# Kernel optimization log

Measured on AMD Instinct MI355X. Metric: run time of the kernel, lower is better.

The kernel has to match this reference:

```python
import jax, jax.numpy as jnp
import numpy as np

N_EMBED = 1024
HIDDEN = int(2 / 3 * 4 * N_EMBED)  # 2730, matches SwiGLU default
NUM_EXPERTS = 8
TOP_K = 2


def setup_inputs() -> dict:
    key = jax.random.key(0)
    ks = jax.random.split(key, 5)
    B, T, C, E, H = 2, 2048, N_EMBED, NUM_EXPERTS, HIDDEN
    s = 0.02
    return {
        "x": jax.random.normal(ks[0], (B, T, C), dtype=jnp.float32),
        "gate_w": jax.random.normal(ks[1], (E, C), dtype=jnp.float32) * s,  # Linear(C->E) weight [out,in]
        "w1": jax.random.normal(ks[2], (E, H, C), dtype=jnp.float32) * s,   # per-expert Linear(C->H)
        "w2": jax.random.normal(ks[3], (E, H, C), dtype=jnp.float32) * s,   # per-expert Linear(C->H)
        "w3": jax.random.normal(ks[4], (E, C, H), dtype=jnp.float32) * s,   # per-expert Linear(H->C)
    }


def reference(x, gate_w, w1, w2, w3):
    B, T, C = x.shape
    E = gate_w.shape[0]
    xt = x.reshape(-1, C)                      # [N, C], N = B*T
    N = xt.shape[0]

    # Router: top-k logits, softmax over the selected logits only
    logits = jnp.einsum("nc,ec->ne", xt, gate_w)          # [N, E]
    top_vals, top_idx = jax.lax.top_k(logits, TOP_K)       # [N, K]
    top_w = jax.nn.softmax(top_vals.astype(jnp.float32), axis=-1).astype(x.dtype)

    # Dense routing-weight matrix [N, E] (top-k indices are distinct per token)
    route = jnp.zeros((N, E), dtype=x.dtype)
    route = route.at[jnp.arange(N)[:, None], top_idx].set(top_w)

    # SwiGLU for all experts, batched over the expert axis (faithful math,
    # vectorized instead of the per-expert Python-loop gather/scatter)
    h1 = jnp.einsum("nc,ehc->enh", xt, w1)                 # [E, N, H]
    h2 = jnp.einsum("nc,ehc->enh", xt, w2)                 # [E, N, H]
    act = jax.nn.silu(h1) * h2                              # [E, N, H]
    expert_out = jnp.einsum("enh,ech->enc", act, w3)       # [E, N, C]

    out = jnp.einsum("ne,enc->nc", route, expert_out)      # weighted combine
    return out.reshape(B, T, C)
```

## Files before the change

### kernel.cpp

```cpp
#include <hip/hip_runtime.h>
#include <hip/hip_bf16.h>
#include <cstdint>
#include <cstddef>

#define TOKENS 4096
#define CDIM   1024
#define HDIM   2730
#define HPAD2  2816
#define NEXP   8
#define NPAIR  (TOKENS * 2)
#define NTB1   (HPAD2 / 64)
#define NTB2   (CDIM / 128)

typedef __bf16 bf16_t;
typedef bf16_t bf16x8 __attribute__((ext_vector_type(8)));
typedef float  f32x4  __attribute__((ext_vector_type(4)));

static __device__ __forceinline__ unsigned short f2bf(float f) {
    union { float f; unsigned int u; } v; v.f = f;
    unsigned int u = v.u;
    return (unsigned short)((u + 0x7FFFu + ((u >> 16) & 1u)) >> 16);
}
static __device__ __forceinline__ unsigned int pack2(float a, float b) {
    return (unsigned int)f2bf(a) | ((unsigned int)f2bf(b) << 16);
}

typedef __attribute__((address_space(3))) unsigned int lds_uint;
typedef const __attribute__((address_space(1))) unsigned int glob_uint;
static __device__ __forceinline__ void gl_lds16(const void* g, void* l) {
    __builtin_amdgcn_global_load_lds((glob_uint*)g, (lds_uint*)l, 16, 0, 0);
}


__global__ void moe_init(int* meta) {
    if (threadIdx.x < 64) meta[threadIdx.x] = 0;
}

__global__ __launch_bounds__(256) void moe_router(
    const float* __restrict__ x, const float* __restrict__ gw,
    int* __restrict__ meta, int* __restrict__ tok_idx, float* __restrict__ tok_w)
{
    int wave = threadIdx.x >> 6;
    int lane = threadIdx.x & 63;
    int t = blockIdx.x * 4 + wave;

    float acc[NEXP];
#pragma unroll
    for (int e = 0; e < NEXP; ++e) acc[e] = 0.f;

    const float4* xr = (const float4*)(x + (size_t)t * CDIM);
#pragma unroll
    for (int it = 0; it < 4; ++it) {
        int c4 = it * 64 + lane;
        float4 xv = xr[c4];
#pragma unroll
        for (int e = 0; e < NEXP; ++e) {
            float4 gv = ((const float4*)(gw + e * CDIM))[c4];
            acc[e] += xv.x * gv.x + xv.y * gv.y + xv.z * gv.z + xv.w * gv.w;
        }
    }
#pragma unroll
    for (int e = 0; e < NEXP; ++e) {
#pragma unroll
        for (int off = 32; off > 0; off >>= 1)
            acc[e] += __shfl_xor(acc[e], off, 64);
    }
    if (lane == 0) {
        int e0 = 0; float v0 = acc[0];
#pragma unroll
        for (int e = 1; e < NEXP; ++e) if (acc[e] > v0) { v0 = acc[e]; e0 = e; }
        int e1 = -1; float v1 = -3.0e38f;
#pragma unroll
        for (int e = 0; e < NEXP; ++e) if (e != e0 && acc[e] > v1) { v1 = acc[e]; e1 = e; }
        float w0 = 1.f / (1.f + __expf(v1 - v0));
        tok_idx[2 * t] = e0; tok_idx[2 * t + 1] = e1;
        tok_w[2 * t] = w0;  tok_w[2 * t + 1] = 1.f - w0;
        atomicAdd(&meta[e0], 1);
        atomicAdd(&meta[e1], 1);
    }
}

__global__ void moe_scan(int* meta) {
    if (threadIdx.x == 0) {
        int s = 0;
        for (int e = 0; e < NEXP; ++e) { meta[8 + e] = s; s += meta[e]; }
        meta[16] = s;
        int nb = 0;
        for (int e = 0; e < NEXP; ++e) {
            int beg = meta[8 + e], end = meta[8 + e] + meta[e];
            for (int m0 = beg; m0 < end; m0 += 128) {
                meta[32 + 2 * nb] = e;
                meta[33 + 2 * nb] = m0;
                ++nb;
            }
        }
        meta[17] = nb;
    }
}

__global__ __launch_bounds__(256) void moe_scatter(
    const int* __restrict__ tok_idx, const float* __restrict__ tok_w, int* meta,
    int* __restrict__ pair_token, float* __restrict__ pair_w)
{
    int t = blockIdx.x * 256 + threadIdx.x;
    if (t >= TOKENS) return;
#pragma unroll
    for (int k = 0; k < 2; ++k) {
        int e = tok_idx[2 * t + k];
        int pos = atomicAdd(&meta[24 + e], 1);
        int slot = meta[8 + e] + pos;
        pair_token[slot] = t;
        pair_w[slot] = tok_w[2 * t + k];
    }
}

__global__ __launch_bounds__(256) void moe_gather(
    const float* __restrict__ x, const int* __restrict__ pair_token,
    unsigned short* __restrict__ Xg)
{
    int base = blockIdx.x * 8;
    int i = threadIdx.x;
#pragma unroll
    for (int r = 0; r < 8; ++r) {
        int row = base + r;
        int t = pair_token[row];
        float4 v = ((const float4*)(x + (size_t)t * CDIM))[i];
        ushort4 o;
        o.x = f2bf(v.x); o.y = f2bf(v.y); o.z = f2bf(v.z); o.w = f2bf(v.w);
        ((ushort4*)(Xg + (size_t)row * CDIM))[i] = o;
    }
}

__global__ __launch_bounds__(256) void conv_w12(
    const float* __restrict__ w1, const float* __restrict__ w2,
    unsigned short* __restrict__ w1b, unsigned short* __restrict__ w2b)
{
    int e = blockIdx.y;
    const float* wsrc = blockIdx.z ? w2 : w1;
    unsigned short* wdst = blockIdx.z ? w2b : w1b;
    int col = threadIdx.x * 4;
#pragma unroll
    for (int r = 0; r < 8; ++r) {
        int row = blockIdx.x * 8 + r;
        unsigned short* dst = wdst + ((size_t)e * HPAD2 + row) * CDIM;
        uint2 pv;
        if (row < HDIM) {
            float4 a = *(const float4*)(wsrc + ((size_t)e * HDIM + row) * CDIM + col);
            pv.x = pack2(a.x, a.y); pv.y = pack2(a.z, a.w);
        } else {
            pv = uint2{0, 0};
        }
        *(uint2*)(dst + col) = pv;
    }
}

__global__ __launch_bounds__(256) void conv_w3(
    const float* __restrict__ w3, unsigned short* __restrict__ w3b)
{
    int e = blockIdx.y;
#pragma unroll
    for (int r = 0; r < 8; ++r) {
        int row = blockIdx.x * 8 + r;
        const float* src = w3 + ((size_t)e * CDIM + row) * HDIM;
        unsigned short* dst = w3b + ((size_t)e * CDIM + row) * HPAD2;
        for (int ch = threadIdx.x; ch < HPAD2 / 8; ch += 256) {
            int h = ch * 8;
            uint4 pv;
            if (h + 8 <= HDIM) {
                float2 a = *(const float2*)(src + h);
                float2 b = *(const float2*)(src + h + 2);
                float2 c = *(const float2*)(src + h + 4);
                float2 d = *(const float2*)(src + h + 6);
                pv.x = pack2(a.x, a.y); pv.y = pack2(b.x, b.y);
                pv.z = pack2(c.x, c.y); pv.w = pack2(d.x, d.y);
            } else if (h < HDIM) {
                float v[8];
#pragma unroll
                for (int q = 0; q < 8; ++q) v[q] = (h + q < HDIM) ? src[h + q] : 0.f;
                pv.x = pack2(v[0], v[1]); pv.y = pack2(v[2], v[3]);
                pv.z = pack2(v[4], v[5]); pv.w = pack2(v[6], v[7]);
            } else {
                pv = uint4{0, 0, 0, 0};
            }
            *(uint4*)(dst + h) = pv;
        }
    }
}

#define SWZ(row, ch) (((row) << 6) + ((((ch) ^ ((row) & 7))) << 3))

__global__ __launch_bounds__(256) void moe_gemm1(
    const unsigned short* __restrict__ Xg,
    const unsigned short* __restrict__ w1b, const unsigned short* __restrict__ w2b,
    const float* __restrict__ pair_w, int* __restrict__ meta,
    unsigned short* __restrict__ act)
{
    __shared__ unsigned short sA[128 * 64];
    __shared__ unsigned short sB1[64 * 64];
    __shared__ unsigned short sB2[64 * 64];
    __shared__ int sTile;

    int tid = threadIdx.x;
    int lane = tid & 63;
    int wv = tid >> 6;
    int wm = wv >> 1, wn = wv & 1;
    int l3 = lane >> 3;
    int srcc = (((lane & 7) ^ l3) << 3);

    int ntile = meta[17] * NTB1;

    for (;;) {
        if (tid == 0) sTile = atomicAdd(&meta[18], 1);
        __syncthreads();
        int t = sTile;
        if (t >= ntile) break;

        int bm = t / NTB1, bn = t - bm * NTB1;
        int e  = meta[32 + 2 * bm];
        int m0 = meta[33 + 2 * bm];
        int mEnd = meta[9 + e];
        int mEndm1 = mEnd - 1;
        int n0 = bn * 64;

        const unsigned short* w1e = w1b + (size_t)e * HPAD2 * CDIM + (size_t)n0 * CDIM;
        const unsigned short* w2e = w2b + (size_t)e * HPAD2 * CDIM + (size_t)n0 * CDIM;

        f32x4 acc1[4][2], acc2[4][2];
#pragma unroll
        for (int i = 0; i < 4; ++i)
#pragma unroll
            for (int j = 0; j < 2; ++j) {
                acc1[i][j] = {0.f, 0.f, 0.f, 0.f};
                acc2[i][j] = {0.f, 0.f, 0.f, 0.f};
            }

        for (int k0 = 0; k0 < CDIM; k0 += 64) {
#pragma unroll
            for (int i_ = 0; i_ < 4; ++i_) {
                int seg = wv * 4 + i_;
                int row = seg * 8 + l3;
                int grow = m0 + row; if (grow > mEndm1) grow = mEndm1;
                gl_lds16(Xg + (size_t)grow * CDIM + k0 + srcc, sA + seg * 512);
            }
#pragma unroll
            for (int i_ = 0; i_ < 2; ++i_) {
                int seg = wv * 2 + i_;
                int row = seg * 8 + l3;
                gl_lds16(w1e + (size_t)row * CDIM + k0 + srcc, sB1 + seg * 512);
                gl_lds16(w2e + (size_t)row * CDIM + k0 + srcc, sB2 + seg * 512);
            }
            asm volatile("s_waitcnt vmcnt(0)" ::: "memory");
            __syncthreads();
#pragma unroll
            for (int ks = 0; ks < 2; ++ks) {
                int kch = ks * 4 + (lane >> 4);
                bf16x8 af[4], b1f[2], b2f[2];
#pragma unroll
                for (int i = 0; i < 4; ++i) {
                    int r = wm * 64 + i * 16 + (lane & 15);
                    af[i] = *(const bf16x8*)(sA + SWZ(r, kch));
                }
#pragma unroll
                for (int j = 0; j < 2; ++j) {
                    int r = wn * 32 + j * 16 + (lane & 15);
                    b1f[j] = *(const bf16x8*)(sB1 + SWZ(r, kch));
                    b2f[j] = *(const bf16x8*)(sB2 + SWZ(r, kch));
                }
#pragma unroll
                for (int i = 0; i < 4; ++i)
#pragma unroll
                    for (int j = 0; j < 2; ++j) {
                        acc1[i][j] = __builtin_amdgcn_mfma_f32_16x16x32_bf16(af[i], b1f[j], acc1[i][j], 0, 0, 0);
                        acc2[i][j] = __builtin_amdgcn_mfma_f32_16x16x32_bf16(af[i], b2f[j], acc2[i][j], 0, 0, 0);
                    }
            }
            __syncthreads();
        }

#pragma unroll
        for (int i = 0; i < 4; ++i) {
            int rbase = m0 + wm * 64 + i * 16 + ((lane >> 4) << 2);
#pragma unroll
            for (int r = 0; r < 4; ++r) {
                int grow = rbase + r;
                if (grow >= mEnd) continue;
                float pw = pair_w[grow];
                size_t rowoff = (size_t)grow * HPAD2;
#pragma unroll
                for (int j = 0; j < 2; ++j) {
                    int gcol = n0 + wn * 32 + j * 16 + (lane & 15);
                    float h1 = acc1[i][j][r], h2 = acc2[i][j][r];
                    float a = (h1 / (1.f + __expf(-h1))) * h2 * pw;
                    act[rowoff + gcol] = f2bf(a);
                }
            }
        }
        __syncthreads();
    }
}

__global__ __launch_bounds__(256) void moe_gemm2(
    const unsigned short* __restrict__ act,
    const unsigned short* __restrict__ w3b,
    int* __restrict__ meta, const int* __restrict__ pair_token,
    float* __restrict__ out)
{
    __shared__ unsigned short sA[128 * 64];
    __shared__ unsigned short sB[128 * 64];
    __shared__ int sTile;

    int tid = threadIdx.x;
    int lane = tid & 63;
    int wv = tid >> 6;
    int wm = wv >> 1, wn = wv & 1;
    int l3 = lane >> 3;
    int srcc = (((lane & 7) ^ l3) << 3);

    int ntile = meta[17] * NTB2;

    for (;;) {
        if (tid == 0) sTile = atomicAdd(&meta[19], 1);
        __syncthreads();
        int t = sTile;
        if (t >= ntile) break;

        int bm = t / NTB2, bn = t - bm * NTB2;
        int e  = meta[32 + 2 * bm];
        int m0 = meta[33 + 2 * bm];
        int mEnd = meta[9 + e];
        int mEndm1 = mEnd - 1;
        int n0 = bn * 128;

        const unsigned short* w3e = w3b + (size_t)e * CDIM * HPAD2 + (size_t)n0 * HPAD2;

        f32x4 acc[4][4];
#pragma unroll
        for (int i = 0; i < 4; ++i)
#pragma unroll
            for (int j = 0; j < 4; ++j) acc[i][j] = {0.f, 0.f, 0.f, 0.f};

        for (int k0 = 0; k0 < HPAD2; k0 += 64) {
#pragma unroll
            for (int i_ = 0; i_ < 4; ++i_) {
                int seg = wv * 4 + i_;
                int row = seg * 8 + l3;
                int grow = m0 + row; if (grow > mEndm1) grow = mEndm1;
                gl_lds16(act + (size_t)grow * HPAD2 + k0 + srcc, sA + seg * 512);
                gl_lds16(w3e + (size_t)row * HPAD2 + k0 + srcc, sB + seg * 512);
            }
            asm volatile("s_waitcnt vmcnt(0)" ::: "memory");
            __syncthreads();
#pragma unroll
            for (int ks = 0; ks < 2; ++ks) {
                int kch = ks * 4 + (lane >> 4);
                bf16x8 af[4], bf[4];
#pragma unroll
                for (int i = 0; i < 4; ++i) {
                    int r = wm * 64 + i * 16 + (lane & 15);
                    af[i] = *(const bf16x8*)(sA + SWZ(r, kch));
                }
#pragma unroll
                for (int j = 0; j < 4; ++j) {
                    int r = wn * 64 + j * 16 + (lane & 15);
                    bf[j] = *(const bf16x8*)(sB + SWZ(r, kch));
                }
#pragma unroll
                for (int i = 0; i < 4; ++i)
#pragma unroll
                    for (int j = 0; j < 4; ++j)
                        acc[i][j] = __builtin_amdgcn_mfma_f32_16x16x32_bf16(af[i], bf[j], acc[i][j], 0, 0, 0);
            }
            __syncthreads();
        }

#pragma unroll
        for (int i = 0; i < 4; ++i) {
            int rbase = m0 + wm * 64 + i * 16 + ((lane >> 4) << 2);
#pragma unroll
            for (int r = 0; r < 4; ++r) {
                int grow = rbase + r;
                if (grow >= mEnd) continue;
                int tok = pair_token[grow];
                float* orow = out + (size_t)tok * CDIM;
#pragma unroll
                for (int j = 0; j < 4; ++j) {
                    int gcol = n0 + wn * 64 + j * 16 + (lane & 15);
                    atomicAdd(orow + gcol, acc[i][j][r]);
                }
            }
        }
        __syncthreads();
    }
}

extern "C" void kernel_launch(void* const* d_in, const int* in_sizes, int n_in,
                              void* d_out, int out_size, void* d_ws, size_t ws_size,
                              hipStream_t stream)
{
    const float* x  = (const float*)d_in[0];
    const float* gw = (const float*)d_in[1];
    const float* w1 = (const float*)d_in[2];
    const float* w2 = (const float*)d_in[3];
    const float* w3 = (const float*)d_in[4];
    float* out = (float*)d_out;

    char* ws = (char*)d_ws;
    size_t off = 0;
    auto alloc = [&](size_t bytes) -> void* {
        off = (off + 255) & ~(size_t)255;
        void* p = ws + off;
        off += bytes;
        return p;
    };
    int*   meta       = (int*)alloc(256 * sizeof(int));
    int*   tok_idx    = (int*)alloc((size_t)NPAIR * sizeof(int));
    float* tok_w      = (float*)alloc((size_t)NPAIR * sizeof(float));
    int*   pair_token = (int*)alloc((size_t)NPAIR * sizeof(int));
    float* pair_w     = (float*)alloc((size_t)NPAIR * sizeof(float));
    unsigned short* Xg  = (unsigned short*)alloc((size_t)NPAIR * CDIM * 2);
    unsigned short* act = (unsigned short*)alloc((size_t)NPAIR * HPAD2 * 2);
    unsigned short* w1b = (unsigned short*)alloc((size_t)NEXP * HPAD2 * CDIM * 2);
    unsigned short* w2b = (unsigned short*)alloc((size_t)NEXP * HPAD2 * CDIM * 2);
    unsigned short* w3b = (unsigned short*)alloc((size_t)NEXP * CDIM * HPAD2 * 2);
    (void)ws_size; (void)in_sizes; (void)n_in;

    hipMemsetAsync(d_out, 0, (size_t)out_size * sizeof(float), stream);

    moe_init<<<1, 64, 0, stream>>>(meta);
    moe_router<<<TOKENS / 4, 256, 0, stream>>>(x, gw, meta, tok_idx, tok_w);
    moe_scan<<<1, 64, 0, stream>>>(meta);
    moe_scatter<<<TOKENS / 256, 256, 0, stream>>>(tok_idx, tok_w, meta, pair_token, pair_w);
    moe_gather<<<NPAIR / 8, 256, 0, stream>>>(x, pair_token, Xg);
    conv_w12<<<dim3(HPAD2 / 8, NEXP, 2), 256, 0, stream>>>(w1, w2, w1b, w2b);
    conv_w3<<<dim3(CDIM / 8, NEXP), 256, 0, stream>>>(w3, w3b);
    moe_gemm1<<<768, 256, 0, stream>>>(Xg, w1b, w2b, pair_w, meta, act);
    moe_gemm2<<<576, 256, 0, stream>>>(act, w3b, meta, pair_token, out);
}
```

Before: 621.4 us.

## Enlarge MoE GEMM tiles to 512-thread blocks with double-buffered LDS staging

```diff
diff --git a/kernel.cpp b/kernel.cpp
--- a/kernel.cpp
+++ b/kernel.cpp
@@ -9,8 +9,10 @@
 #define HPAD2  2816
 #define NEXP   8
 #define NPAIR  (TOKENS * 2)
-#define NTB1   (HPAD2 / 64)
+#define NTB1   (HPAD2 / 128)
 #define NTB2   (CDIM / 128)
+#define NT1    (CDIM / 64)
+#define NT2    (HPAD2 / 64)
 
 typedef __bf16 bf16_t;
 typedef bf16_t bf16x8 __attribute__((ext_vector_type(8)));
@@ -85,16 +87,26 @@
         int s = 0;
         for (int e = 0; e < NEXP; ++e) { meta[8 + e] = s; s += meta[e]; }
         meta[16] = s;
-        int nb = 0;
+        int nb1 = 0;
+        for (int e = 0; e < NEXP; ++e) {
+            int beg = meta[8 + e], end = meta[8 + e] + meta[e];
+            for (int m0 = beg; m0 < end; m0 += 256) {
+                meta[32 + 2 * nb1] = e;
+                meta[33 + 2 * nb1] = m0;
+                ++nb1;
+            }
+        }
+        meta[17] = nb1;
+        int nb2 = 0;
         for (int e = 0; e < NEXP; ++e) {
             int beg = meta[8 + e], end = meta[8 + e] + meta[e];
             for (int m0 = beg; m0 < end; m0 += 128) {
-                meta[32 + 2 * nb] = e;
-                meta[33 + 2 * nb] = m0;
-                ++nb;
-            }
-        }
-        meta[17] = nb;
+                meta[128 + 2 * nb2] = e;
+                meta[129 + 2 * nb2] = m0;
+                ++nb2;
+            }
+        }
+        meta[20] = nb2;
     }
 }
 
@@ -189,21 +201,20 @@
 
 #define SWZ(row, ch) (((row) << 6) + ((((ch) ^ ((row) & 7))) << 3))
 
-__global__ __launch_bounds__(256) void moe_gemm1(
+__global__ __launch_bounds__(512, 2) void moe_gemm1(
     const unsigned short* __restrict__ Xg,
     const unsigned short* __restrict__ w1b, const unsigned short* __restrict__ w2b,
     const float* __restrict__ pair_w, int* __restrict__ meta,
     unsigned short* __restrict__ act)
 {
-    __shared__ unsigned short sA[128 * 64];
-    __shared__ unsigned short sB1[64 * 64];
-    __shared__ unsigned short sB2[64 * 64];
+    __shared__ unsigned short sA[2][256 * 64];
+    __shared__ unsigned short sB[2][256 * 64];
     __shared__ int sTile;
 
     int tid = threadIdx.x;
     int lane = tid & 63;
     int wv = tid >> 6;
-    int wm = wv >> 1, wn = wv & 1;
+    int wm = wv >> 2, wn = wv & 3;
     int l3 = lane >> 3;
     int srcc = (((lane & 7) ^ l3) << 3);
 
@@ -220,54 +231,57 @@
         int m0 = meta[33 + 2 * bm];
         int mEnd = meta[9 + e];
         int mEndm1 = mEnd - 1;
-        int n0 = bn * 64;
+        int n0 = bn * 128;
 
         const unsigned short* w1e = w1b + (size_t)e * HPAD2 * CDIM + (size_t)n0 * CDIM;
         const unsigned short* w2e = w2b + (size_t)e * HPAD2 * CDIM + (size_t)n0 * CDIM;
-
-        f32x4 acc1[4][2], acc2[4][2];
-#pragma unroll
-        for (int i = 0; i < 4; ++i)
+        const unsigned short* bbase = (wv < 4) ? w1e : w2e;
+
+        f32x4 acc1[8][2], acc2[8][2];
+#pragma unroll
+        for (int i = 0; i < 8; ++i)
 #pragma unroll
             for (int j = 0; j < 2; ++j) {
                 acc1[i][j] = {0.f, 0.f, 0.f, 0.f};
                 acc2[i][j] = {0.f, 0.f, 0.f, 0.f};
             }
 
-        for (int k0 = 0; k0 < CDIM; k0 += 64) {
+        auto STAGE = [&](int b, int kk) {
+            int k0 = kk * 64;
 #pragma unroll
             for (int i_ = 0; i_ < 4; ++i_) {
                 int seg = wv * 4 + i_;
-                int row = seg * 8 + l3;
-                int grow = m0 + row; if (grow > mEndm1) grow = mEndm1;
-                gl_lds16(Xg + (size_t)grow * CDIM + k0 + srcc, sA + seg * 512);
-            }
-#pragma unroll
-            for (int i_ = 0; i_ < 2; ++i_) {
-                int seg = wv * 2 + i_;
-                int row = seg * 8 + l3;
-                gl_lds16(w1e + (size_t)row * CDIM + k0 + srcc, sB1 + seg * 512);
-                gl_lds16(w2e + (size_t)row * CDIM + k0 + srcc, sB2 + seg * 512);
-            }
-            asm volatile("s_waitcnt vmcnt(0)" ::: "memory");
-            __syncthreads();
+                int arow = seg * 8 + l3;
+                int grow = m0 + arow; if (grow > mEndm1) grow = mEndm1;
+                gl_lds16(Xg + (size_t)grow * CDIM + k0 + srcc, sA[b] + seg * 512);
+                int bseg = (wv < 4) ? seg : seg - 16;
+                gl_lds16(bbase + (size_t)(bseg * 8 + l3) * CDIM + k0 + srcc, sB[b] + seg * 512);
+            }
+        };
+
+        STAGE(0, 0);
+        __syncthreads();
+        for (int t_ = 0; t_ < NT1; ++t_) {
+            int cur = t_ & 1;
+            if (t_ + 1 < NT1) STAGE(cur ^ 1, t_ + 1);
 #pragma unroll
             for (int ks = 0; ks < 2; ++ks) {
                 int kch = ks * 4 + (lane >> 4);
-                bf16x8 af[4], b1f[2], b2f[2];
-#pragma unroll
-                for (int i = 0; i < 4; ++i) {
-                    int r = wm * 64 + i * 16 + (lane & 15);
-                    af[i] = *(const bf16x8*)(sA + SWZ(r, kch));
+                bf16x8 af[8], b1f[2], b2f[2];
+#pragma unroll
+                for (int i = 0; i < 8; ++i) {
+                    int r = wm * 128 + i * 16 + (lane & 15);
+                    af[i] = *(const bf16x8*)(sA[cur] + SWZ(r, kch));
                 }
 #pragma unroll
                 for (int j = 0; j < 2; ++j) {
-                    int r = wn * 32 + j * 16 + (lane & 15);
-                    b1f[j] = *(const bf16x8*)(sB1 + SWZ(r, kch));
-                    b2f[j] = *(const bf16x8*)(sB2 + SWZ(r, kch));
-                }
-#pragma unroll
-                for (int i = 0; i < 4; ++i)
+                    int r1 = wn * 32 + j * 16 + (lane & 15);
+                    b1f[j] = *(const bf16x8*)(sB[cur] + SWZ(r1, kch));
+                    int r2 = 128 + r1;
+                    b2f[j] = *(const bf16x8*)(sB[cur] + SWZ(r2, kch));
+                }
+#pragma unroll
+                for (int i = 0; i < 8; ++i)
 #pragma unroll
                     for (int j = 0; j < 2; ++j) {
                         acc1[i][j] = __builtin_amdgcn_mfma_f32_16x16x32_bf16(af[i], b1f[j], acc1[i][j], 0, 0, 0);
@@ -278,8 +292,8 @@
         }
 
 #pragma unroll
-        for (int i = 0; i < 4; ++i) {
-            int rbase = m0 + wm * 64 + i * 16 + ((lane >> 4) << 2);
+        for (int i = 0; i < 8; ++i) {
+            int rbase = m0 + wm * 128 + i * 16 + ((lane >> 4) << 2);
 #pragma unroll
             for (int r = 0; r < 4; ++r) {
                 int grow = rbase + r;
@@ -295,28 +309,27 @@
                 }
             }
         }
-        __syncthreads();
-    }
-}
-
-__global__ __launch_bounds__(256) void moe_gemm2(
+    }
+}
+
+__global__ __launch_bounds__(512, 2) void moe_gemm2(
     const unsigned short* __restrict__ act,
     const unsigned short* __restrict__ w3b,
     int* __restrict__ meta, const int* __restrict__ pair_token,
     float* __restrict__ out)
 {
-    __shared__ unsigned short sA[128 * 64];
-    __shared__ unsigned short sB[128 * 64];
+    __shared__ unsigned short sA[2][128 * 64];
+    __shared__ unsigned short sB[2][128 * 64];
     __shared__ int sTile;
 
     int tid = threadIdx.x;
     int lane = tid & 63;
     int wv = tid >> 6;
-    int wm = wv >> 1, wn = wv & 1;
+    int wm = wv >> 2, wn = wv & 3;
     int l3 = lane >> 3;
     int srcc = (((lane & 7) ^ l3) << 3);
 
-    int ntile = meta[17] * NTB2;
+    int ntile = meta[20] * NTB2;
 
     for (;;) {
         if (tid == 0) sTile = atomicAdd(&meta[19], 1);
@@ -325,49 +338,55 @@
         if (t >= ntile) break;
 
         int bm = t / NTB2, bn = t - bm * NTB2;
-        int e  = meta[32 + 2 * bm];
-        int m0 = meta[33 + 2 * bm];
+        int e  = meta[128 + 2 * bm];
+        int m0 = meta[129 + 2 * bm];
         int mEnd = meta[9 + e];
         int mEndm1 = mEnd - 1;
         int n0 = bn * 128;
 
         const unsigned short* w3e = w3b + (size_t)e * CDIM * HPAD2 + (size_t)n0 * HPAD2;
 
-        f32x4 acc[4][4];
+        f32x4 acc[4][2];
 #pragma unroll
         for (int i = 0; i < 4; ++i)
 #pragma unroll
-            for (int j = 0; j < 4; ++j) acc[i][j] = {0.f, 0.f, 0.f, 0.f};
-
-        for (int k0 = 0; k0 < HPAD2; k0 += 64) {
-#pragma unroll
-            for (int i_ = 0; i_ < 4; ++i_) {
-                int seg = wv * 4 + i_;
+            for (int j = 0; j < 2; ++j) acc[i][j] = {0.f, 0.f, 0.f, 0.f};
+
+        auto STAGE = [&](int b, int kk) {
+            int k0 = kk * 64;
+#pragma unroll
+            for (int i_ = 0; i_ < 2; ++i_) {
+                int seg = wv * 2 + i_;
                 int row = seg * 8 + l3;
                 int grow = m0 + row; if (grow > mEndm1) grow = mEndm1;
-                gl_lds16(act + (size_t)grow * HPAD2 + k0 + srcc, sA + seg * 512);
-                gl_lds16(w3e + (size_t)row * HPAD2 + k0 + srcc, sB + seg * 512);
-            }
-            asm volatile("s_waitcnt vmcnt(0)" ::: "memory");
-            __syncthreads();
+                gl_lds16(act + (size_t)grow * HPAD2 + k0 + srcc, sA[b] + seg * 512);
+                gl_lds16(w3e + (size_t)row * HPAD2 + k0 + srcc, sB[b] + seg * 512);
+            }
+        };
+
+        STAGE(0, 0);
+        __syncthreads();
+        for (int t_ = 0; t_ < NT2; ++t_) {
+            int cur = t_ & 1;
+            if (t_ + 1 < NT2) STAGE(cur ^ 1, t_ + 1);
 #pragma unroll
             for (int ks = 0; ks < 2; ++ks) {
                 int kch = ks * 4 + (lane >> 4);
-                bf16x8 af[4], bf[4];
+                bf16x8 af[4], bf[2];
 #pragma unroll
                 for (int i = 0; i < 4; ++i) {
                     int r = wm * 64 + i * 16 + (lane & 15);
-                    af[i] = *(const bf16x8*)(sA + SWZ(r, kch));
-                }
-#pragma unroll
-                for (int j = 0; j < 4; ++j) {
-                    int r = wn * 64 + j * 16 + (lane & 15);
-                    bf[j] = *(const bf16x8*)(sB + SWZ(r, kch));
+                    af[i] = *(const bf16x8*)(sA[cur] + SWZ(r, kch));
+                }
+#pragma unroll
+                for (int j = 0; j < 2; ++j) {
+                    int r = wn * 32 + j * 16 + (lane & 15);
+                    bf[j] = *(const bf16x8*)(sB[cur] + SWZ(r, kch));
                 }
 #pragma unroll
                 for (int i = 0; i < 4; ++i)
 #pragma unroll
-                    for (int j = 0; j < 4; ++j)
+                    for (int j = 0; j < 2; ++j)
                         acc[i][j] = __builtin_amdgcn_mfma_f32_16x16x32_bf16(af[i], bf[j], acc[i][j], 0, 0, 0);
             }
             __syncthreads();
@@ -383,13 +402,12 @@
                 int tok = pair_token[grow];
                 float* orow = out + (size_t)tok * CDIM;
 #pragma unroll
-                for (int j = 0; j < 4; ++j) {
-                    int gcol = n0 + wn * 64 + j * 16 + (lane & 15);
+                for (int j = 0; j < 2; ++j) {
+                    int gcol = n0 + wn * 32 + j * 16 + (lane & 15);
                     atomicAdd(orow + gcol, acc[i][j][r]);
                 }
             }
         }
-        __syncthreads();
     }
 }
 
@@ -412,7 +430,7 @@
         off += bytes;
         return p;
     };
-    int*   meta       = (int*)alloc(256 * sizeof(int));
+    int*   meta       = (int*)alloc(512 * sizeof(int));
     int*   tok_idx    = (int*)alloc((size_t)NPAIR * sizeof(int));
     float* tok_w      = (float*)alloc((size_t)NPAIR * sizeof(float));
     int*   pair_token = (int*)alloc((size_t)NPAIR * sizeof(int));
@@ -433,6 +451,6 @@
     moe_gather<<<NPAIR / 8, 256, 0, stream>>>(x, pair_token, Xg);
     conv_w12<<<dim3(HPAD2 / 8, NEXP, 2), 256, 0, stream>>>(w1, w2, w1b, w2b);
     conv_w3<<<dim3(CDIM / 8, NEXP), 256, 0, stream>>>(w3, w3b);
-    moe_gemm1<<<768, 256, 0, stream>>>(Xg, w1b, w2b, pair_w, meta, act);
-    moe_gemm2<<<576, 256, 0, stream>>>(act, w3b, meta, pair_token, out);
-}
+    moe_gemm1<<<256, 512, 0, stream>>>(Xg, w1b, w2b, pair_w, meta, act);
+    moe_gemm2<<<512, 512, 0, stream>>>(act, w3b, meta, pair_token, out);
+}
```

Result: faster. 516.6 us (-16.9%).
